# Optimization experiments

Measured on AMD Instinct MI355X. Metric: run time of the kernel, lower is better.

Reference implementation:

```python
import jax, jax.numpy as jnp
import numpy as np

N = 40000      # num nodes
M = 640000     # num edges (avg degree 16)
D = 128        # hidden_size / embed_dim
H = 8          # attn_num_heads
HD = D // H    # head_dim = 16
FF = 512       # tfmr_ff_sz
LN_EPS = 1e-5
SOFTMAX_EPS = 1e-16  # matches torch_geometric.utils.softmax


def setup_inputs() -> dict:
    key = jax.random.key(0)
    ks = jax.random.split(key, 8)
    s = 0.05
    return {
        "node_states": jax.random.normal(ks[0], (N, D), dtype=jnp.float32),
        "edges": jax.random.randint(ks[1], (2, M), 0, N, dtype=jnp.int64),
        # SelfAttentionMessageLayer params (F.linear convention: W is (out, in))
        "w_qkv": jax.random.normal(ks[2], (3 * D, D), dtype=jnp.float32) * s,
        "b_qkv": jnp.zeros((3 * D,), dtype=jnp.float32),
        "w_out": jax.random.normal(ks[3], (D, D), dtype=jnp.float32) * s,
        "b_out": jnp.zeros((D,), dtype=jnp.float32),
        # TransformerUpdateLayer params
        "w1": jax.random.normal(ks[4], (FF, D), dtype=jnp.float32) * s,
        "b1": jnp.zeros((FF,), dtype=jnp.float32),
        "w2": jax.random.normal(ks[5], (D, FF), dtype=jnp.float32) * s,
        "b2": jnp.zeros((D,), dtype=jnp.float32),
        "g1": jnp.ones((D,), dtype=jnp.float32),
        "beta1": jnp.zeros((D,), dtype=jnp.float32),
        "g2": jnp.ones((D,), dtype=jnp.float32),
        "beta2": jnp.zeros((D,), dtype=jnp.float32),
    }


def _layer_norm(x, g, b):
    mu = jnp.mean(x, axis=-1, keepdims=True)
    var = jnp.mean(jnp.square(x - mu), axis=-1, keepdims=True)
    return g * (x - mu) * jax.lax.rsqrt(var + LN_EPS) + b


def _sparse_self_attention(node_states, edges, w_qkv, b_qkv, w_out, b_out):
    num_nodes = node_states.shape[0]
    src, tgt = edges[0], edges[1]
    qkv = node_states @ w_qkv.T + b_qkv                      # (N, 3D)
    q, k, v = jnp.split(qkv, 3, axis=1)                      # each (N, D)
    q_e = q[tgt]                                             # (M, D) gather by target
    k_e = k[src]                                             # (M, D) gather by source
    v_e = v[src]                                             # (M, D)
    m = q_e.shape[0]
    # per-edge, per-head scaled dot-product scores
    scores = (q_e * k_e).reshape(m, H, HD).sum(-1) * (HD ** -0.5)   # (M, H)
    # scatter-softmax over edges sharing the same target node
    smax = jax.ops.segment_max(scores, tgt, num_segments=num_nodes)  # (N, H)
    smax = jnp.where(jnp.isfinite(smax), smax, 0.0)                  # empty segments
    ex = jnp.exp(scores - smax[tgt])                                 # (M, H)
    ssum = jax.ops.segment_sum(ex, tgt, num_segments=num_nodes)      # (N, H)
    attn_w = ex / (ssum[tgt] + SOFTMAX_EPS)                          # (M, H)
    # weighted scatter-add aggregation
    msg = (v_e.reshape(m, H, HD) * attn_w[:, :, None]).reshape(m, D)  # (M, D)
    agg = jax.ops.segment_sum(msg, tgt, num_segments=num_nodes)      # (N, D)
    return agg @ w_out.T + b_out


def _update(messages, node_states, w1, b1, w2, b2, g1, beta1, g2, beta2):
    x = _layer_norm(node_states + messages, g1, beta1)
    ff = jax.nn.relu(x @ w1.T + b1) @ w2.T + b2
    return _layer_norm(x + ff, g2, beta2)


def reference(node_states, edges, w_qkv, b_qkv, w_out, b_out,
              w1, b1, w2, b2, g1, beta1, g2, beta2):
    old_node_states = node_states
    # layer_timesteps = [1]: one message/update layer, one propagation step
    messages = _sparse_self_attention(node_states, edges, w_qkv, b_qkv, w_out, b_out)
    node_states = _update(messages, node_states, w1, b1, w2, b2, g1, beta1, g2, beta2)
    return (node_states, old_node_states)
```

## Files before the change

### kernel.cpp

```cpp
#include <hip/hip_runtime.h>
#include <hip/hip_bf16.h>
#include <math.h>

#define D_DIM 128
#define FF_DIM 512
#define BSTRIDE 64
#define BCAP 63
#define PSHIFT 6
#define NBINS 625
#define CAP_BIN 1280
#define P1_EPB 4096

typedef __attribute__((ext_vector_type(8))) short bf16x8;
typedef __attribute__((ext_vector_type(4))) float f32x4;
typedef __attribute__((ext_vector_type(2))) float f32x2;
typedef __attribute__((ext_vector_type(4))) unsigned short u16x4;

__device__ __forceinline__ short f2bf(float f) {
    union { float f; unsigned u; } x; x.f = f;
    unsigned r = x.u + 0x7FFF + ((x.u >> 16) & 1);
    return (short)(r >> 16);
}
__device__ __forceinline__ float bf2f(short s) {
    union { unsigned u; float f; } x;
    x.u = ((unsigned)(unsigned short)s) << 16;
    return x.f;
}
__device__ __forceinline__ float lof(unsigned u) {
    union { unsigned u; float f; } x; x.u = u << 16; return x.f;
}
__device__ __forceinline__ float hif(unsigned u) {
    union { unsigned u; float f; } x; x.u = u & 0xFFFF0000u; return x.f;
}
__device__ __forceinline__ unsigned char f2fp8(float v) {
    return (unsigned char)(__builtin_amdgcn_cvt_pk_fp8_f32(v, v, 0, false) & 0xFF);
}

__device__ __forceinline__ void load_lds16(const short* g, short* l) {
    __builtin_amdgcn_global_load_lds(
        (const __attribute__((address_space(1))) unsigned int*)g,
        (__attribute__((address_space(3))) unsigned int*)l, 16, 0, 0);
}

template<int OUT_BF16, int RELU>
__global__ __launch_bounds__(256) void gemm_mfma(
    const short* __restrict__ A, const short* __restrict__ B,
    const float* __restrict__ bias, void* __restrict__ C,
    int Nc, int K)
{
    __shared__ short lA[2][128 * 32];
    __shared__ short lB[2][128 * 32];

    const int tid  = threadIdx.x;
    const int lane = tid & 63;
    const int wave = tid >> 6;
    const int wr = wave >> 1, wc = wave & 1;
    const int row0 = blockIdx.y * 128;
    const int col0 = blockIdx.x * 128;
    const int fr = lane & 15;
    const int fq = lane >> 4;
    const int sw = (fr >> 1) & 3;
    const int rdoff = (fq ^ sw) * 8;

    const int c0c = tid,        r0 = c0c >> 2, qg0 = (c0c & 3) ^ ((r0 >> 1) & 3);
    const int c1c = 256 + tid,  r1 = c1c >> 2, qg1 = (c1c & 3) ^ ((r1 >> 1) & 3);

#define STAGE_G(buf, kk) { \
    load_lds16(A + (size_t)(row0 + r0) * K + (kk) + qg0 * 8, &lA[buf][c0c * 8]); \
    load_lds16(B + (size_t)(col0 + r0) * K + (kk) + qg0 * 8, &lB[buf][c0c * 8]); \
    load_lds16(A + (size_t)(row0 + r1) * K + (kk) + qg1 * 8, &lA[buf][c1c * 8]); \
    load_lds16(B + (size_t)(col0 + r1) * K + (kk) + qg1 * 8, &lB[buf][c1c * 8]); }

    f32x4 acc[4][4] = {};
    const int nk = K >> 5;

    STAGE_G(0, 0)
    __syncthreads();
    int cur = 0;
    for (int t = 0; t < nk; ++t) {
        if (t + 1 < nk) STAGE_G(cur ^ 1, (t + 1) * 32)

        bf16x8 af[4], bfr[4];
#pragma unroll
        for (int m = 0; m < 4; ++m)
            af[m] = *(const bf16x8*)&lA[cur][(wr * 64 + m * 16 + fr) * 32 + rdoff];
#pragma unroll
        for (int n2 = 0; n2 < 4; ++n2)
            bfr[n2] = *(const bf16x8*)&lB[cur][(wc * 64 + n2 * 16 + fr) * 32 + rdoff];
#pragma unroll
        for (int m = 0; m < 4; ++m)
#pragma unroll
            for (int n2 = 0; n2 < 4; ++n2)
                acc[m][n2] = __builtin_amdgcn_mfma_f32_16x16x32_bf16(
                    af[m], bfr[n2], acc[m][n2], 0, 0, 0);
        __syncthreads();
        cur ^= 1;
    }
#undef STAGE_G

#pragma unroll
    for (int m = 0; m < 4; ++m) {
        int r = row0 + wr * 64 + m * 16 + fq * 4;
#pragma unroll
        for (int n2 = 0; n2 < 4; ++n2) {
            int c = col0 + wc * 64 + n2 * 16 + fr;
            float bb = bias[c];
#pragma unroll
            for (int j = 0; j < 4; ++j) {
                float v = acc[m][n2][j] + bb;
                if (RELU) v = fmaxf(v, 0.0f);
                if (OUT_BF16)
                    ((short*)C)[(size_t)(r + j) * Nc + c] = f2bf(v);
                else
                    ((float*)C)[(size_t)(r + j) * Nc + c] = v;
            }
        }
    }
}

__global__ __launch_bounds__(256) void qkv_bucket(
    const short* __restrict__ A, const short* __restrict__ B,
    const float* __restrict__ bias, void* __restrict__ C, int K,
    const unsigned* __restrict__ part, const int* __restrict__ gcur,
    int* __restrict__ csr, int ngemm)
{
    __shared__ short lA[2][128 * 32];
    __shared__ short lB[2][128 * 32];
    __shared__ int lbkt[64 * BSTRIDE];
    __shared__ int lcnt[64];

    const int b = blockIdx.x;
    const int tid = threadIdx.x;

    if (b >= ngemm) {
        int bin = b - ngemm;
        for (int i = tid; i < 64; i += 256) lcnt[i] = 0;
        __syncthreads();
        int cnt = gcur[bin]; if (cnt > CAP_BIN) cnt = CAP_BIN;
        const unsigned* pp = part + (size_t)bin * CAP_BIN;
        for (int i = tid; i < cnt; i += 256) {
            unsigned pk = pp[i];
            int lt = (pk >> 16) & 63;
            int s  = pk & 0xFFFF;
            int pos = atomicAdd(&lcnt[lt], 1);
            if (pos < BCAP) lbkt[lt * BSTRIDE + 1 + pos] = s;
        }
        __syncthreads();
        for (int i = tid; i < 64; i += 256) lbkt[i * BSTRIDE] = lcnt[i];
        __syncthreads();
        int4* dst = (int4*)(csr + (size_t)bin * 64 * BSTRIDE);
        const int4* sp = (const int4*)lbkt;
        for (int i = tid; i < 64 * BSTRIDE / 4; i += 256) dst[i] = sp[i];
        return;
    }

    const int lane = tid & 63;
    const int wave = tid >> 6;
    const int wr = wave >> 1, wc = wave & 1;
    const int row0 = (b / 3) * 128;
    const int col0 = (b % 3) * 128;
    const int fr = lane & 15;
    const int fq = lane >> 4;
    const int sw = (fr >> 1) & 3;
    const int rdoff = (fq ^ sw) * 8;

    const int c0c = tid,        r0 = c0c >> 2, qg0 = (c0c & 3) ^ ((r0 >> 1) & 3);
    const int c1c = 256 + tid,  r1 = c1c >> 2, qg1 = (c1c & 3) ^ ((r1 >> 1) & 3);

#define STAGE_Q(buf, kk) { \
    load_lds16(A + (size_t)(row0 + r0) * K + (kk) + qg0 * 8, &lA[buf][c0c * 8]); \
    load_lds16(B + (size_t)(col0 + r0) * K + (kk) + qg0 * 8, &lB[buf][c0c * 8]); \
    load_lds16(A + (size_t)(row0 + r1) * K + (kk) + qg1 * 8, &lA[buf][c1c * 8]); \
    load_lds16(B + (size_t)(col0 + r1) * K + (kk) + qg1 * 8, &lB[buf][c1c * 8]); }

    f32x4 acc[4][4] = {};
    const int nk = K >> 5;

    STAGE_Q(0, 0)
    __syncthreads();
    int cur = 0;
    for (int t = 0; t < nk; ++t) {
        if (t + 1 < nk) STAGE_Q(cur ^ 1, (t + 1) * 32)

        bf16x8 af[4], bfr[4];
#pragma unroll
        for (int m = 0; m < 4; ++m)
            af[m] = *(const bf16x8*)&lA[cur][(wr * 64 + m * 16 + fr) * 32 + rdoff];
#pragma unroll
        for (int n2 = 0; n2 < 4; ++n2)
            bfr[n2] = *(const bf16x8*)&lB[cur][(wc * 64 + n2 * 16 + fr) * 32 + rdoff];
#pragma unroll
        for (int m = 0; m < 4; ++m)
#pragma unroll
            for (int n2 = 0; n2 < 4; ++n2)
                acc[m][n2] = __builtin_amdgcn_mfma_f32_16x16x32_bf16(
                    af[m], bfr[n2], acc[m][n2], 0, 0, 0);
        __syncthreads();
        cur ^= 1;
    }
#undef STAGE_Q

#pragma unroll
    for (int m = 0; m < 4; ++m) {
        int r = row0 + wr * 64 + m * 16 + fq * 4;
#pragma unroll
        for (int n2 = 0; n2 < 4; ++n2) {
            int c = col0 + wc * 64 + n2 * 16 + fr;
            float bb = bias[c];
#pragma unroll
            for (int j = 0; j < 4; ++j) {
                float v = acc[m][n2][j] + bb;
                if (col0 == 0) {
                    ((short*)C)[(size_t)(r + j) * 256 + c] = f2bf(v);
                } else {
                    size_t byteoff = (size_t)(r + j) * 512 +
                        (col0 == 128 ? 256 + (c - 128) : 384 + (c - 256));
                    ((unsigned char*)C)[byteoff] = f2fp8(v);
                }
            }
        }
    }
}

template<int KD, int RES_BF, int OUT_BF>
__global__ __launch_bounds__(256) void gemm_ln(
    const short* __restrict__ A, const short* __restrict__ B,
    const float* __restrict__ bias, const void* __restrict__ res,
    const float* __restrict__ gamma, const float* __restrict__ beta,
    float* __restrict__ out32, short* __restrict__ outbf, int n)
{
    __shared__ short lA[2][64 * 32];
    __shared__ short lB[2][128 * 32];
    __shared__ float sums[64][2], sqs[64][2];
    __shared__ float muA[64], rsA[64];

    const int tid  = threadIdx.x;
    const int lane = tid & 63;
    const int wave = tid >> 6;
    const int wr = wave >> 1, wc = wave & 1;
    const int row0 = blockIdx.x * 64;
    const int fr = lane & 15;
    const int fq = lane >> 4;
    const int sw = (fr >> 1) & 3;
    const int rdoff = (fq ^ sw) * 8;

    const int ra = tid >> 2,        qa = (tid & 3) ^ ((ra >> 1) & 3);
    const int cb0 = tid,       rb0 = cb0 >> 2, qb0 = (cb0 & 3) ^ ((rb0 >> 1) & 3);
    const int cb1 = 256 + tid, rb1 = cb1 >> 2, qb1 = (cb1 & 3) ^ ((rb1 >> 1) & 3);

#define STAGE_L(buf, kk) { \
    load_lds16(A + (size_t)(row0 + ra) * KD + (kk) + qa * 8,  &lA[buf][tid * 8]); \
    load_lds16(B + (size_t)rb0 * KD + (kk) + qb0 * 8, &lB[buf][cb0 * 8]); \
    load_lds16(B + (size_t)rb1 * KD + (kk) + qb1 * 8, &lB[buf][cb1 * 8]); }

    f32x4 acc[2][4] = {};
    const int nk = KD >> 5;

    STAGE_L(0, 0)
    __syncthreads();
    int cur = 0;
    for (int t = 0; t < nk; ++t) {
        if (t + 1 < nk) STAGE_L(cur ^ 1, (t + 1) * 32)

        bf16x8 af[2], bfr[4];
#pragma unroll
        for (int m = 0; m < 2; ++m)
            af[m] = *(const bf16x8*)&lA[cur][(wr * 32 + m * 16 + fr) * 32 + rdoff];
#pragma unroll
        for (int n2 = 0; n2 < 4; ++n2)
            bfr[n2] = *(const bf16x8*)&lB[cur][(wc * 64 + n2 * 16 + fr) * 32 + rdoff];
#pragma unroll
        for (int m = 0; m < 2; ++m)
#pragma unroll
            for (int n2 = 0; n2 < 4; ++n2)
                acc[m][n2] = __builtin_amdgcn_mfma_f32_16x16x32_bf16(
                    af[m], bfr[n2], acc[m][n2], 0, 0, 0);
        __syncthreads();
        cur ^= 1;
    }
#undef STAGE_L

    float bicol[4], gcol[4], bcol[4];
#pragma unroll
    for (int n2 = 0; n2 < 4; ++n2) {
        int c = wc * 64 + n2 * 16 + fr;
        bicol[n2] = bias[c]; gcol[n2] = gamma[c]; bcol[n2] = beta[c];
    }

#pragma unroll
    for (int m = 0; m < 2; ++m) {
#pragma unroll
        for (int j = 0; j < 4; ++j) {
            int rl = wr * 32 + m * 16 + fq * 4 + j;
            int rg = row0 + rl;
            float ps = 0.0f, pq = 0.0f;
#pragma unroll
            for (int n2 = 0; n2 < 4; ++n2) {
                float v = acc[m][n2][j] + bicol[n2];
                if (rg < n) {
                    size_t ri = (size_t)rg * 128 + wc * 64 + n2 * 16 + fr;
                    v += RES_BF ? bf2f(((const short*)res)[ri])
                                : ((const float*)res)[ri];
                }
                acc[m][n2][j] = v;
                ps += v; pq += v * v;
            }
            ps += __shfl_xor(ps, 1); ps += __shfl_xor(ps, 2);
            ps += __shfl_xor(ps, 4); ps += __shfl_xor(ps, 8);
            pq += __shfl_xor(pq, 1); pq += __shfl_xor(pq, 2);
            pq += __shfl_xor(pq, 4); pq += __shfl_xor(pq, 8);
            if (fr == 0) { sums[rl][wc] = ps; sqs[rl][wc] = pq; }
        }
    }
    __syncthreads();
    if (tid < 64) {
        float s = sums[tid][0] + sums[tid][1];
        float q = sqs[tid][0] + sqs[tid][1];
        float mu = s * (1.0f / 128.0f);
        float var = q * (1.0f / 128.0f) - mu * mu;
        muA[tid] = mu;
        rsA[tid] = rsqrtf(var + 1e-5f);
    }
    __syncthreads();

#pragma unroll
    for (int m = 0; m < 2; ++m) {
#pragma unroll
        for (int j = 0; j < 4; ++j) {
            int rl = wr * 32 + m * 16 + fq * 4 + j;
            int rg = row0 + rl;
            float mu = muA[rl], rs = rsA[rl];
#pragma unroll
            for (int n2 = 0; n2 < 4; ++n2) {
                int c = wc * 64 + n2 * 16 + fr;
                float o = gcol[n2] * (acc[m][n2][j] - mu) * rs + bcol[n2];
                if (OUT_BF) {
                    outbf[(size_t)rg * 128 + c] = (rg < n) ? f2bf(o) : (short)0;
                } else {
                    if (rg < n) out32[(size_t)rg * 128 + c] = o;
                }
            }
        }
    }
}

__global__ __launch_bounds__(256) void prep_kernel(
    const float* __restrict__ ns, short* __restrict__ nsbf,
    float* __restrict__ out_old, int n_elems, int mp_elems,
    const float* w0, const float* w1, const float* w2, const float* w3,
    short* o0, short* o1, short* o2, short* o3,
    int c0, int c1, int c2, int c3,
    const int* __restrict__ e_src, const int* __restrict__ e_tgt,
    int* __restrict__ gcur, unsigned* __restrict__ part,
    int m_edges, int nconv)
{
    __shared__ int hist[NBINS];
    __shared__ int base[NBINS];

    const int tid = threadIdx.x;

    if (blockIdx.x >= nconv) {
        int pblk = blockIdx.x - nconv;
        int e0 = pblk * P1_EPB;
        for (int i = tid; i < NBINS; i += 256) hist[i] = 0;
        __syncthreads();
        unsigned packs[16]; int bins[16];
#pragma unroll
        for (int j = 0; j < 16; ++j) {
            int i = e0 + j * 256 + tid;
            if (i < m_edges) {
                int t = e_tgt[i], s = e_src[i];
                packs[j] = ((unsigned)t << 16) | (unsigned)s;
                bins[j] = t >> PSHIFT;
                atomicAdd(&hist[bins[j]], 1);
            } else { bins[j] = -1; packs[j] = 0u; }
        }
        __syncthreads();
        for (int i = tid; i < NBINS; i += 256) {
            int c = hist[i];
            base[i] = c ? atomicAdd(&gcur[i], c) : 0;
            hist[i] = 0;
        }
        __syncthreads();
#pragma unroll
        for (int j = 0; j < 16; ++j) {
            if (bins[j] >= 0) {
                int pos = base[bins[j]] + atomicAdd(&hist[bins[j]], 1);
                if (pos < CAP_BIN)
                    part[(size_t)bins[j] * CAP_BIN + pos] = packs[j];
            }
        }
        return;
    }

    int i = blockIdx.x * 256 + tid;
    int i4 = i * 4;
    if (i4 < mp_elems) {
        if (i4 < n_elems) {
            float4 v = *(const float4*)(ns + i4);
            *(float4*)(out_old + i4) = v;
            u16x4 b;
            b.x = (unsigned short)f2bf(v.x); b.y = (unsigned short)f2bf(v.y);
            b.z = (unsigned short)f2bf(v.z); b.w = (unsigned short)f2bf(v.w);
            *(u16x4*)(nsbf + i4) = b;
        } else {
            u16x4 z = {0, 0, 0, 0};
            *(u16x4*)(nsbf + i4) = z;
        }
    }
    if (i < c0) o0[i] = f2bf(w0[i]);
    if (i < c1) o1[i] = f2bf(w1[i]);
    if (i < c2) o2[i] = f2bf(w2[i]);
    if (i < c3) o3[i] = f2bf(w3[i]);
}

template<int NG>
__device__ __forceinline__ void attn_fast(
    int cnt, int e, int mysrc,
    const unsigned char* kb, const unsigned char* vb,
    f32x2 q01, f32x2 q23, f32x2 q45, f32x2 q67,
    float& l, f32x2& A01, f32x2& A23, f32x2& A45, f32x2& A67)
{
    uint2 kr[NG]; float sc[NG]; int si[NG];
#pragma unroll
    for (int G = 0; G < NG; ++G) {
        if (4 * G < cnt) {
            int idx = 4 * G + e; if (idx >= cnt) idx = cnt - 1;
            si[G] = __shfl(mysrc, idx);
            kr[G] = *(const uint2*)(kb + (size_t)si[G] * 512);
        }
    }
    float mloc = -INFINITY;
#pragma unroll
    for (int G = 0; G < NG; ++G) {
        if (4 * G < cnt) {
            f32x2 s2 = q01 * __builtin_amdgcn_cvt_pk_f32_fp8(kr[G].x, 0);
            s2 += q23 * __builtin_amdgcn_cvt_pk_f32_fp8(kr[G].x, 1);
            s2 += q45 * __builtin_amdgcn_cvt_pk_f32_fp8(kr[G].y, 0);
            s2 += q67 * __builtin_amdgcn_cvt_pk_f32_fp8(kr[G].y, 1);
            float s = s2.x + s2.y;
            s += __shfl_xor(s, 4);
            sc[G] = (4 * G + e < cnt) ? s : -INFINITY;
            mloc = fmaxf(mloc, sc[G]);
        }
    }
    mloc = fmaxf(mloc, __shfl_xor(mloc, 1));
    mloc = fmaxf(mloc, __shfl_xor(mloc, 2));
#pragma unroll
    for (int G = 0; G < NG; ++G) {
        if (4 * G < cnt) {
            float p = exp2f(sc[G] - mloc);
            sc[G] = p;
            l += p;
        }
    }
    uint2 vr[NG];
#pragma unroll
    for (int G = 0; G < NG; ++G) {
        if (4 * G < cnt)
            vr[G] = *(const uint2*)(vb + (size_t)si[G] * 512);
    }
#pragma unroll
    for (int G = 0; G < NG; ++G) {
        if (4 * G < cnt) {
            f32x2 pv = {sc[G], sc[G]};
            A01 += pv * __builtin_amdgcn_cvt_pk_f32_fp8(vr[G].x, 0);
            A23 += pv * __builtin_amdgcn_cvt_pk_f32_fp8(vr[G].x, 1);
            A45 += pv * __builtin_amdgcn_cvt_pk_f32_fp8(vr[G].y, 0);
            A67 += pv * __builtin_amdgcn_cvt_pk_f32_fp8(vr[G].y, 1);
        }
    }
}

__global__ __launch_bounds__(256) void attn_kernel(
    const short* __restrict__ qkv, const int* __restrict__ csr,
    short* __restrict__ agg, int n, int mp)
{
    int node = blockIdx.x * 4 + (threadIdx.x >> 6);
    int lane = threadIdx.x & 63;
    if (node >= mp) return;
    const int hh = lane >> 2;
    const int e  = lane & 3;
    unsigned* outp = (unsigned*)(agg + (size_t)node * 128 + hh * 8 + e * 2);

    const int* bkt = csr + (size_t)node * BSTRIDE;
    int cnt = 0;
    if (node < n) {
        cnt = bkt[0];
        if (cnt > BCAP) cnt = BCAP;
    }
    if (cnt == 0) { *outp = 0u; return; }

    const float SC = 0.25f * 1.44269504088896340736f;
    const uint4 qd = *(const uint4*)(qkv + (size_t)node * 256 + hh * 8);
    f32x2 q01 = {lof(qd.x) * SC, hif(qd.x) * SC};
    f32x2 q23 = {lof(qd.y) * SC, hif(qd.y) * SC};
    f32x2 q45 = {lof(qd.z) * SC, hif(qd.z) * SC};
    f32x2 q67 = {lof(qd.w) * SC, hif(qd.w) * SC};

    const unsigned char* kb = (const unsigned char*)qkv + 256 + hh * 8;
    const unsigned char* vb = (const unsigned char*)qkv + 384 + hh * 8;

    float l = 0.0f;
    f32x2 A01 = {0, 0}, A23 = {0, 0}, A45 = {0, 0}, A67 = {0, 0};

    int mysrc = bkt[1 + ((lane < cnt) ? lane : (cnt - 1))];

    if (cnt <= 16) {
        attn_fast<4>(cnt, e, mysrc, kb, vb, q01, q23, q45, q67,
                     l, A01, A23, A45, A67);
    } else if (cnt <= 32) {
        attn_fast<8>(cnt, e, mysrc, kb, vb, q01, q23, q45, q67,
                     l, A01, A23, A45, A67);
    } else {
        float m = -INFINITY;
        uint2 kA, vA;
        {
            int sA = bkt[1 + ((e < cnt) ? e : 0)];
            kA = *(const uint2*)(kb + (size_t)sA * 512);
            vA = *(const uint2*)(vb + (size_t)sA * 512);
        }
        for (int g = 0; g < cnt; g += 4) {
            uint2 kB = kA, vB = vA;
            if (g + 4 < cnt) {
                int t = g + 4 + e;
                int sB = bkt[1 + ((t < cnt) ? t : 0)];
                kB = *(const uint2*)(kb + (size_t)sB * 512);
                vB = *(const uint2*)(vb + (size_t)sB * 512);
            }
            f32x2 s2 = q01 * __builtin_amdgcn_cvt_pk_f32_fp8(kA.x, 0);
            s2 += q23 * __builtin_amdgcn_cvt_pk_f32_fp8(kA.x, 1);
            s2 += q45 * __builtin_amdgcn_cvt_pk_f32_fp8(kA.y, 0);
            s2 += q67 * __builtin_amdgcn_cvt_pk_f32_fp8(kA.y, 1);
            float s = s2.x + s2.y;
            s += __shfl_xor(s, 4);
            float scv = (g + e < cnt) ? s : -INFINITY;
            float gm = fmaxf(scv, __shfl_xor(scv, 1));
            gm = fmaxf(gm, __shfl_xor(gm, 2));
            float mnew = fmaxf(m, gm);
            float corr = exp2f(m - mnew);
            float p = exp2f(scv - mnew);
            l = fmaf(l, corr, p);
            f32x2 cv = {corr, corr}, pv = {p, p};
            A01 = A01 * cv + pv * __builtin_amdgcn_cvt_pk_f32_fp8(vA.x, 0);
            A23 = A23 * cv + pv * __builtin_amdgcn_cvt_pk_f32_fp8(vA.x, 1);
            A45 = A45 * cv + pv * __builtin_amdgcn_cvt_pk_f32_fp8(vA.y, 0);
            A67 = A67 * cv + pv * __builtin_amdgcn_cvt_pk_f32_fp8(vA.y, 1);
            m = mnew;
            kA = kB; vA = vB;
        }
    }

    float a0 = A01.x, a1 = A01.y, a2 = A23.x, a3 = A23.y;
    float a4 = A45.x, a5 = A45.y, a6 = A67.x, a7 = A67.y;

    l  += __shfl_xor(l, 1);
    a0 += __shfl_xor(a0, 1); a1 += __shfl_xor(a1, 1);
    a2 += __shfl_xor(a2, 1); a3 += __shfl_xor(a3, 1);
    a4 += __shfl_xor(a4, 1); a5 += __shfl_xor(a5, 1);
    a6 += __shfl_xor(a6, 1); a7 += __shfl_xor(a7, 1);
    l  += __shfl_xor(l, 2);
    a0 += __shfl_xor(a0, 2); a1 += __shfl_xor(a1, 2);
    a2 += __shfl_xor(a2, 2); a3 += __shfl_xor(a3, 2);
    a4 += __shfl_xor(a4, 2); a5 += __shfl_xor(a5, 2);
    a6 += __shfl_xor(a6, 2); a7 += __shfl_xor(a7, 2);

    float inv = 1.0f / l;
    float o0, o1;
    if (e == 0)      { o0 = a0; o1 = a1; }
    else if (e == 1) { o0 = a2; o1 = a3; }
    else if (e == 2) { o0 = a4; o1 = a5; }
    else             { o0 = a6; o1 = a7; }
    *outp = ((unsigned)(unsigned short)f2bf(o1 * inv) << 16) |
            (unsigned)(unsigned short)f2bf(o0 * inv);
}

extern "C" void kernel_launch(void* const* d_in, const int* in_sizes, int n_in,
                              void* d_out, int out_size, void* d_ws, size_t ws_size,
                              hipStream_t stream)
{
    const float* node_states = (const float*)d_in[0];
    const int*   edges       = (const int*)d_in[1];
    const float* w_qkv = (const float*)d_in[2];
    const float* b_qkv = (const float*)d_in[3];
    const float* w_out = (const float*)d_in[4];
    const float* b_out = (const float*)d_in[5];
    const float* w1    = (const float*)d_in[6];
    const float* b1    = (const float*)d_in[7];
    const float* w2    = (const float*)d_in[8];
    const float* b2    = (const float*)d_in[9];
    const float* g1    = (const float*)d_in[10];
    const float* beta1 = (const float*)d_in[11];
    const float* g2    = (const float*)d_in[12];
    const float* beta2 = (const float*)d_in[13];

    const int N  = in_sizes[0] / D_DIM;
    const int M  = in_sizes[1] / 2;
    const int MP = ((N + 127) / 128) * 128;
    const int* e_src = edges;
    const int* e_tgt = edges + M;

    float* out_new = (float*)d_out;
    float* out_old = (float*)d_out + (size_t)N * D_DIM;

    size_t off = 0;
    auto alloc = [&](size_t bytes) -> void* {
        void* p = (char*)d_ws + off;
        off += (bytes + 255) & ~(size_t)255;
        return p;
    };
    short* ns_bf   = (short*)alloc((size_t)MP * D_DIM * 2);
    char*  region  = (char*)alloc((size_t)MP * 512);
    short* qkv_pk  = (short*)region;
    short* xbuf_bf = (short*)region;
    short* agg_bf  = (short*)alloc((size_t)MP * D_DIM * 2);
    short* ff1_bf  = (short*)alloc((size_t)MP * FF_DIM * 2);
    short* wqkv_bf = (short*)alloc((size_t)384 * 128 * 2);
    short* wout_bf = (short*)alloc((size_t)128 * 128 * 2);
    short* w1_bf   = (short*)alloc((size_t)512 * 128 * 2);
    short* w2_bf   = (short*)alloc((size_t)128 * 512 * 2);
    int* csr       = (int*)alloc((size_t)N * BSTRIDE * 4);
    unsigned* part = (unsigned*)alloc((size_t)NBINS * CAP_BIN * 4);
    int* gcur      = (int*)alloc((size_t)NBINS * 4);
    (void)ws_size;

    hipMemsetAsync(gcur, 0, (size_t)NBINS * 4, stream);

    const int nconv = (MP * D_DIM / 4 + 255) / 256;
    const int nP1   = (M + P1_EPB - 1) / P1_EPB;
    prep_kernel<<<nconv + nP1, 256, 0, stream>>>(
        node_states, ns_bf, out_old, N * D_DIM, MP * D_DIM,
        w_qkv, w_out, w1, w2, wqkv_bf, wout_bf, w1_bf, w2_bf,
        384 * 128, 128 * 128, 512 * 128, 128 * 512,
        e_src, e_tgt, gcur, part, M, nconv);

    {
        const int ngemm = 3 * (MP / 128);
        qkv_bucket<<<ngemm + NBINS, 256, 0, stream>>>(
            ns_bf, wqkv_bf, b_qkv, qkv_pk, 128,
            part, gcur, csr, ngemm);
    }
    attn_kernel<<<MP / 4, 256, 0, stream>>>(qkv_pk, csr, agg_bf, N, MP);
    gemm_ln<128, 1, 1><<<MP / 64, 256, 0, stream>>>(
        agg_bf, wout_bf, b_out, ns_bf, g1, beta1,
        (float*)nullptr, xbuf_bf, N);
    {
        dim3 grid(FF_DIM / 128, MP / 128);
        gemm_mfma<1, 1><<<grid, 256, 0, stream>>>(xbuf_bf, w1_bf, b1,
                                                  ff1_bf, FF_DIM, 128);
    }
    gemm_ln<512, 1, 0><<<MP / 64, 256, 0, stream>>>(
        ff1_bf, w2_bf, b2, xbuf_bf, g2, beta2, out_new, (short*)nullptr, N);
}
```

Measured before the change: 149.7 us.

## Fuse out-projection+LayerNorm with FF1 GEMM and split Q/KV buffers

Merges the W_out GEMM + residual + LayerNorm kernel with the following FF1 GEMM+ReLU. The normalized rows are kept in a swizzled LDS tile and multiplied by W1, which is read directly from global memory. This removes one kernel launch and the global read of the intermediate x buffer. It also splits the packed QKV buffer into a bf16 Q array and a compact 256-byte-stride fp8 K/V array, so attention gathers touch denser rows. The cost is extra LDS per block and unstaged W1 fragment loads from global/L2.

```diff
diff --git a/kernel.cpp b/kernel.cpp
--- a/kernel.cpp
+++ b/kernel.cpp
@@ -42,85 +42,10 @@
         (__attribute__((address_space(3))) unsigned int*)l, 16, 0, 0);
 }
 
-template<int OUT_BF16, int RELU>
-__global__ __launch_bounds__(256) void gemm_mfma(
-    const short* __restrict__ A, const short* __restrict__ B,
-    const float* __restrict__ bias, void* __restrict__ C,
-    int Nc, int K)
-{
-    __shared__ short lA[2][128 * 32];
-    __shared__ short lB[2][128 * 32];
-
-    const int tid  = threadIdx.x;
-    const int lane = tid & 63;
-    const int wave = tid >> 6;
-    const int wr = wave >> 1, wc = wave & 1;
-    const int row0 = blockIdx.y * 128;
-    const int col0 = blockIdx.x * 128;
-    const int fr = lane & 15;
-    const int fq = lane >> 4;
-    const int sw = (fr >> 1) & 3;
-    const int rdoff = (fq ^ sw) * 8;
-
-    const int c0c = tid,        r0 = c0c >> 2, qg0 = (c0c & 3) ^ ((r0 >> 1) & 3);
-    const int c1c = 256 + tid,  r1 = c1c >> 2, qg1 = (c1c & 3) ^ ((r1 >> 1) & 3);
-
-#define STAGE_G(buf, kk) { \
-    load_lds16(A + (size_t)(row0 + r0) * K + (kk) + qg0 * 8, &lA[buf][c0c * 8]); \
-    load_lds16(B + (size_t)(col0 + r0) * K + (kk) + qg0 * 8, &lB[buf][c0c * 8]); \
-    load_lds16(A + (size_t)(row0 + r1) * K + (kk) + qg1 * 8, &lA[buf][c1c * 8]); \
-    load_lds16(B + (size_t)(col0 + r1) * K + (kk) + qg1 * 8, &lB[buf][c1c * 8]); }
-
-    f32x4 acc[4][4] = {};
-    const int nk = K >> 5;
-
-    STAGE_G(0, 0)
-    __syncthreads();
-    int cur = 0;
-    for (int t = 0; t < nk; ++t) {
-        if (t + 1 < nk) STAGE_G(cur ^ 1, (t + 1) * 32)
-
-        bf16x8 af[4], bfr[4];
-#pragma unroll
-        for (int m = 0; m < 4; ++m)
-            af[m] = *(const bf16x8*)&lA[cur][(wr * 64 + m * 16 + fr) * 32 + rdoff];
-#pragma unroll
-        for (int n2 = 0; n2 < 4; ++n2)
-            bfr[n2] = *(const bf16x8*)&lB[cur][(wc * 64 + n2 * 16 + fr) * 32 + rdoff];
-#pragma unroll
-        for (int m = 0; m < 4; ++m)
-#pragma unroll
-            for (int n2 = 0; n2 < 4; ++n2)
-                acc[m][n2] = __builtin_amdgcn_mfma_f32_16x16x32_bf16(
-                    af[m], bfr[n2], acc[m][n2], 0, 0, 0);
-        __syncthreads();
-        cur ^= 1;
-    }
-#undef STAGE_G
-
-#pragma unroll
-    for (int m = 0; m < 4; ++m) {
-        int r = row0 + wr * 64 + m * 16 + fq * 4;
-#pragma unroll
-        for (int n2 = 0; n2 < 4; ++n2) {
-            int c = col0 + wc * 64 + n2 * 16 + fr;
-            float bb = bias[c];
-#pragma unroll
-            for (int j = 0; j < 4; ++j) {
-                float v = acc[m][n2][j] + bb;
-                if (RELU) v = fmaxf(v, 0.0f);
-                if (OUT_BF16)
-                    ((short*)C)[(size_t)(r + j) * Nc + c] = f2bf(v);
-                else
-                    ((float*)C)[(size_t)(r + j) * Nc + c] = v;
-            }
-        }
-    }
-}
-
 __global__ __launch_bounds__(256) void qkv_bucket(
     const short* __restrict__ A, const short* __restrict__ B,
-    const float* __restrict__ bias, void* __restrict__ C, int K,
+    const float* __restrict__ bias, short* __restrict__ Q,
+    unsigned char* __restrict__ KV, int K,
     const unsigned* __restrict__ part, const int* __restrict__ gcur,
     int* __restrict__ csr, int ngemm)
 {
@@ -211,28 +136,30 @@
             for (int j = 0; j < 4; ++j) {
                 float v = acc[m][n2][j] + bb;
                 if (col0 == 0) {
-                    ((short*)C)[(size_t)(r + j) * 256 + c] = f2bf(v);
+                    Q[(size_t)(r + j) * 128 + c] = f2bf(v);
+                } else if (col0 == 128) {
+                    KV[(size_t)(r + j) * 256 + (c - 128)] = f2fp8(v);
                 } else {
-                    size_t byteoff = (size_t)(r + j) * 512 +
-                        (col0 == 128 ? 256 + (c - 128) : 384 + (c - 256));
-                    ((unsigned char*)C)[byteoff] = f2fp8(v);
+                    KV[(size_t)(r + j) * 256 + 128 + (c - 256)] = f2fp8(v);
                 }
             }
         }
     }
 }
 
-template<int KD, int RES_BF, int OUT_BF>
-__global__ __launch_bounds__(256) void gemm_ln(
+__global__ __launch_bounds__(256) void wout_ln_ff1(
     const short* __restrict__ A, const short* __restrict__ B,
-    const float* __restrict__ bias, const void* __restrict__ res,
+    const float* __restrict__ bias, const short* __restrict__ res,
     const float* __restrict__ gamma, const float* __restrict__ beta,
-    float* __restrict__ out32, short* __restrict__ outbf, int n)
+    short* __restrict__ outbf,
+    const short* __restrict__ W1, const float* __restrict__ b1,
+    short* __restrict__ ff1, int n)
 {
     __shared__ short lA[2][64 * 32];
     __shared__ short lB[2][128 * 32];
     __shared__ float sums[64][2], sqs[64][2];
     __shared__ float muA[64], rsA[64];
+    __shared__ short xl[64 * 128];
 
     const int tid  = threadIdx.x;
     const int lane = tid & 63;
@@ -249,18 +176,17 @@
     const int cb1 = 256 + tid, rb1 = cb1 >> 2, qb1 = (cb1 & 3) ^ ((rb1 >> 1) & 3);
 
 #define STAGE_L(buf, kk) { \
-    load_lds16(A + (size_t)(row0 + ra) * KD + (kk) + qa * 8,  &lA[buf][tid * 8]); \
-    load_lds16(B + (size_t)rb0 * KD + (kk) + qb0 * 8, &lB[buf][cb0 * 8]); \
-    load_lds16(B + (size_t)rb1 * KD + (kk) + qb1 * 8, &lB[buf][cb1 * 8]); }
+    load_lds16(A + (size_t)(row0 + ra) * 128 + (kk) + qa * 8,  &lA[buf][tid * 8]); \
+    load_lds16(B + (size_t)rb0 * 128 + (kk) + qb0 * 8, &lB[buf][cb0 * 8]); \
+    load_lds16(B + (size_t)rb1 * 128 + (kk) + qb1 * 8, &lB[buf][cb1 * 8]); }
 
     f32x4 acc[2][4] = {};
-    const int nk = KD >> 5;
 
     STAGE_L(0, 0)
     __syncthreads();
     int cur = 0;
-    for (int t = 0; t < nk; ++t) {
-        if (t + 1 < nk) STAGE_L(cur ^ 1, (t + 1) * 32)
+    for (int t = 0; t < 4; ++t) {
+        if (t + 1 < 4) STAGE_L(cur ^ 1, (t + 1) * 32)
 
         bf16x8 af[2], bfr[4];
 #pragma unroll
@@ -297,11 +223,8 @@
 #pragma unroll
             for (int n2 = 0; n2 < 4; ++n2) {
                 float v = acc[m][n2][j] + bicol[n2];
-                if (rg < n) {
-                    size_t ri = (size_t)rg * 128 + wc * 64 + n2 * 16 + fr;
-                    v += RES_BF ? bf2f(((const short*)res)[ri])
-                                : ((const float*)res)[ri];
-                }
+                if (rg < n)
+                    v += bf2f(res[(size_t)rg * 128 + wc * 64 + n2 * 16 + fr]);
                 acc[m][n2][j] = v;
                 ps += v; pq += v * v;
             }
@@ -334,11 +257,166 @@
             for (int n2 = 0; n2 < 4; ++n2) {
                 int c = wc * 64 + n2 * 16 + fr;
                 float o = gcol[n2] * (acc[m][n2][j] - mu) * rs + bcol[n2];
-                if (OUT_BF) {
-                    outbf[(size_t)rg * 128 + c] = (rg < n) ? f2bf(o) : (short)0;
-                } else {
-                    if (rg < n) out32[(size_t)rg * 128 + c] = o;
+                short ob = (rg < n) ? f2bf(o) : (short)0;
+                outbf[(size_t)rg * 128 + c] = ob;
+                int c8s = ((c >> 3) ^ (rl & 7));
+                xl[rl * 128 + (c8s << 3) + (c & 7)] = ob;
+            }
+        }
+    }
+    __syncthreads();
+
+    for (int cc = 0; cc < 4; ++cc) {
+        const int c0 = wc * 256 + cc * 64;
+        f32x4 a2[2][4] = {};
+#pragma unroll
+        for (int ks = 0; ks < 4; ++ks) {
+            int k0 = ks * 32;
+            bf16x8 af[2], bfr[4];
+#pragma unroll
+            for (int m = 0; m < 2; ++m) {
+                int row = wr * 32 + m * 16 + fr;
+                int ch = ((k0 >> 3) + fq) ^ (row & 7);
+                af[m] = *(const bf16x8*)&xl[row * 128 + (ch << 3)];
+            }
+#pragma unroll
+            for (int n2 = 0; n2 < 4; ++n2)
+                bfr[n2] = *(const bf16x8*)(W1 + (size_t)(c0 + n2 * 16 + fr) * 128
+                                              + k0 + fq * 8);
+#pragma unroll
+            for (int m = 0; m < 2; ++m)
+#pragma unroll
+                for (int n2 = 0; n2 < 4; ++n2)
+                    a2[m][n2] = __builtin_amdgcn_mfma_f32_16x16x32_bf16(
+                        af[m], bfr[n2], a2[m][n2], 0, 0, 0);
+        }
+#pragma unroll
+        for (int m = 0; m < 2; ++m) {
+#pragma unroll
+            for (int n2 = 0; n2 < 4; ++n2) {
+                int c = c0 + n2 * 16 + fr;
+                float bb = b1[c];
+#pragma unroll
+                for (int j = 0; j < 4; ++j) {
+                    int rg = row0 + wr * 32 + m * 16 + fq * 4 + j;
+                    float v = fmaxf(a2[m][n2][j] + bb, 0.0f);
+                    ff1[(size_t)rg * 512 + c] = f2bf(v);
                 }
+            }
+        }
+    }
+}
+
+template<int KD>
+__global__ __launch_bounds__(256) void gemm_ln(
+    const short* __restrict__ A, const short* __restrict__ B,
+    const float* __restrict__ bias, const short* __restrict__ res,
+    const float* __restrict__ gamma, const float* __restrict__ beta,
+    float* __restrict__ out32, int n)
+{
+    __shared__ short lA[2][64 * 32];
+    __shared__ short lB[2][128 * 32];
+    __shared__ float sums[64][2], sqs[64][2];
+    __shared__ float muA[64], rsA[64];
+
+    const int tid  = threadIdx.x;
+    const int lane = tid & 63;
+    const int wave = tid >> 6;
+    const int wr = wave >> 1, wc = wave & 1;
+    const int row0 = blockIdx.x * 64;
+    const int fr = lane & 15;
+    const int fq = lane >> 4;
+    const int sw = (fr >> 1) & 3;
+    const int rdoff = (fq ^ sw) * 8;
+
+    const int ra = tid >> 2,        qa = (tid & 3) ^ ((ra >> 1) & 3);
+    const int cb0 = tid,       rb0 = cb0 >> 2, qb0 = (cb0 & 3) ^ ((rb0 >> 1) & 3);
+    const int cb1 = 256 + tid, rb1 = cb1 >> 2, qb1 = (cb1 & 3) ^ ((rb1 >> 1) & 3);
+
+#define STAGE_L(buf, kk) { \
+    load_lds16(A + (size_t)(row0 + ra) * KD + (kk) + qa * 8,  &lA[buf][tid * 8]); \
+    load_lds16(B + (size_t)rb0 * KD + (kk) + qb0 * 8, &lB[buf][cb0 * 8]); \
+    load_lds16(B + (size_t)rb1 * KD + (kk) + qb1 * 8, &lB[buf][cb1 * 8]); }
+
+    f32x4 acc[2][4] = {};
+    const int nk = KD >> 5;
+
+    STAGE_L(0, 0)
+    __syncthreads();
+    int cur = 0;
+    for (int t = 0; t < nk; ++t) {
+        if (t + 1 < nk) STAGE_L(cur ^ 1, (t + 1) * 32)
+
+        bf16x8 af[2], bfr[4];
+#pragma unroll
+        for (int m = 0; m < 2; ++m)
+            af[m] = *(const bf16x8*)&lA[cur][(wr * 32 + m * 16 + fr) * 32 + rdoff];
+#pragma unroll
+        for (int n2 = 0; n2 < 4; ++n2)
+            bfr[n2] = *(const bf16x8*)&lB[cur][(wc * 64 + n2 * 16 + fr) * 32 + rdoff];
+#pragma unroll
+        for (int m = 0; m < 2; ++m)
+#pragma unroll
+            for (int n2 = 0; n2 < 4; ++n2)
+                acc[m][n2] = __builtin_amdgcn_mfma_f32_16x16x32_bf16(
+                    af[m], bfr[n2], acc[m][n2], 0, 0, 0);
+        __syncthreads();
+        cur ^= 1;
+    }
+#undef STAGE_L
+
+    float bicol[4], gcol[4], bcol[4];
+#pragma unroll
+    for (int n2 = 0; n2 < 4; ++n2) {
+        int c = wc * 64 + n2 * 16 + fr;
+        bicol[n2] = bias[c]; gcol[n2] = gamma[c]; bcol[n2] = beta[c];
+    }
+
+#pragma unroll
+    for (int m = 0; m < 2; ++m) {
+#pragma unroll
+        for (int j = 0; j < 4; ++j) {
+            int rl = wr * 32 + m * 16 + fq * 4 + j;
+            int rg = row0 + rl;
+            float ps = 0.0f, pq = 0.0f;
+#pragma unroll
+            for (int n2 = 0; n2 < 4; ++n2) {
+                float v = acc[m][n2][j] + bicol[n2];
+                if (rg < n)
+                    v += bf2f(res[(size_t)rg * 128 + wc * 64 + n2 * 16 + fr]);
+                acc[m][n2][j] = v;
+                ps += v; pq += v * v;
+            }
+            ps += __shfl_xor(ps, 1); ps += __shfl_xor(ps, 2);
+            ps += __shfl_xor(ps, 4); ps += __shfl_xor(ps, 8);
+            pq += __shfl_xor(pq, 1); pq += __shfl_xor(pq, 2);
+            pq += __shfl_xor(pq, 4); pq += __shfl_xor(pq, 8);
+            if (fr == 0) { sums[rl][wc] = ps; sqs[rl][wc] = pq; }
+        }
+    }
+    __syncthreads();
+    if (tid < 64) {
+        float s = sums[tid][0] + sums[tid][1];
+        float q = sqs[tid][0] + sqs[tid][1];
+        float mu = s * (1.0f / 128.0f);
+        float var = q * (1.0f / 128.0f) - mu * mu;
+        muA[tid] = mu;
+        rsA[tid] = rsqrtf(var + 1e-5f);
+    }
+    __syncthreads();
+
+#pragma unroll
+    for (int m = 0; m < 2; ++m) {
+#pragma unroll
+        for (int j = 0; j < 4; ++j) {
+            int rl = wr * 32 + m * 16 + fq * 4 + j;
+            int rg = row0 + rl;
+            float mu = muA[rl], rs = rsA[rl];
+#pragma unroll
+            for (int n2 = 0; n2 < 4; ++n2) {
+                int c = wc * 64 + n2 * 16 + fr;
+                float o = gcol[n2] * (acc[m][n2][j] - mu) * rs + bcol[n2];
+                if (rg < n) out32[(size_t)rg * 128 + c] = o;
             }
         }
     }
@@ -427,7 +505,7 @@
         if (4 * G < cnt) {
             int idx = 4 * G + e; if (idx >= cnt) idx = cnt - 1;
             si[G] = __shfl(mysrc, idx);
-            kr[G] = *(const uint2*)(kb + (size_t)si[G] * 512);
+            kr[G] = *(const uint2*)(kb + (size_t)si[G] * 256);
         }
     }
     float mloc = -INFINITY;
@@ -458,7 +536,7 @@
 #pragma unroll
     for (int G = 0; G < NG; ++G) {
         if (4 * G < cnt)
-            vr[G] = *(const uint2*)(vb + (size_t)si[G] * 512);
+            vr[G] = *(const uint2*)(vb + (size_t)si[G] * 256);
     }
 #pragma unroll
     for (int G = 0; G < NG; ++G) {
@@ -473,8 +551,8 @@
 }
 
 __global__ __launch_bounds__(256) void attn_kernel(
-    const short* __restrict__ qkv, const int* __restrict__ csr,
-    short* __restrict__ agg, int n, int mp)
+    const short* __restrict__ qb, const unsigned char* __restrict__ kv8,
+    const int* __restrict__ csr, short* __restrict__ agg, int n, int mp)
 {
     int node = blockIdx.x * 4 + (threadIdx.x >> 6);
     int lane = threadIdx.x & 63;
@@ -492,14 +570,14 @@
     if (cnt == 0) { *outp = 0u; return; }
 
     const float SC = 0.25f * 1.44269504088896340736f;
-    const uint4 qd = *(const uint4*)(qkv + (size_t)node * 256 + hh * 8);
+    const uint4 qd = *(const uint4*)(qb + (size_t)node * 128 + hh * 8);
     f32x2 q01 = {lof(qd.x) * SC, hif(qd.x) * SC};
     f32x2 q23 = {lof(qd.y) * SC, hif(qd.y) * SC};
     f32x2 q45 = {lof(qd.z) * SC, hif(qd.z) * SC};
     f32x2 q67 = {lof(qd.w) * SC, hif(qd.w) * SC};
 
-    const unsigned char* kb = (const unsigned char*)qkv + 256 + hh * 8;
-    const unsigned char* vb = (const unsigned char*)qkv + 384 + hh * 8;
+    const unsigned char* kb = kv8 + hh * 8;
+    const unsigned char* vb = kv8 + 128 + hh * 8;
 
     float l = 0.0f;
     f32x2 A01 = {0, 0}, A23 = {0, 0}, A45 = {0, 0}, A67 = {0, 0};
@@ -517,16 +595,16 @@
         uint2 kA, vA;
         {
             int sA = bkt[1 + ((e < cnt) ? e : 0)];
-            kA = *(const uint2*)(kb + (size_t)sA * 512);
-            vA = *(const uint2*)(vb + (size_t)sA * 512);
+            kA = *(const uint2*)(kb + (size_t)sA * 256);
+            vA = *(const uint2*)(vb + (size_t)sA * 256);
         }
         for (int g = 0; g < cnt; g += 4) {
             uint2 kB = kA, vB = vA;
             if (g + 4 < cnt) {
                 int t = g + 4 + e;
                 int sB = bkt[1 + ((t < cnt) ? t : 0)];
-                kB = *(const uint2*)(kb + (size_t)sB * 512);
-                vB = *(const uint2*)(vb + (size_t)sB * 512);
+                kB = *(const uint2*)(kb + (size_t)sB * 256);
+                vB = *(const uint2*)(vb + (size_t)sB * 256);
             }
             f32x2 s2 = q01 * __builtin_amdgcn_cvt_pk_f32_fp8(kA.x, 0);
             s2 += q23 * __builtin_amdgcn_cvt_pk_f32_fp8(kA.x, 1);
@@ -610,9 +688,9 @@
         return p;
     };
     short* ns_bf   = (short*)alloc((size_t)MP * D_DIM * 2);
-    char*  region  = (char*)alloc((size_t)MP * 512);
-    short* qkv_pk  = (short*)region;
-    short* xbuf_bf = (short*)region;
+    short* qb      = (short*)alloc((size_t)MP * D_DIM * 2);
+    short* xbuf_bf = qb;
+    unsigned char* kv8 = (unsigned char*)alloc((size_t)MP * 256);
     short* agg_bf  = (short*)alloc((size_t)MP * D_DIM * 2);
     short* ff1_bf  = (short*)alloc((size_t)MP * FF_DIM * 2);
     short* wqkv_bf = (short*)alloc((size_t)384 * 128 * 2);
@@ -637,18 +715,13 @@
     {
         const int ngemm = 3 * (MP / 128);
         qkv_bucket<<<ngemm + NBINS, 256, 0, stream>>>(
-            ns_bf, wqkv_bf, b_qkv, qkv_pk, 128,
+            ns_bf, wqkv_bf, b_qkv, qb, kv8, 128,
             part, gcur, csr, ngemm);
     }
-    attn_kernel<<<MP / 4, 256, 0, stream>>>(qkv_pk, csr, agg_bf, N, MP);
-    gemm_ln<128, 1, 1><<<MP / 64, 256, 0, stream>>>(
-        agg_bf, wout_bf, b_out, ns_bf, g1, beta1,
-        (float*)nullptr, xbuf_bf, N);
-    {
-        dim3 grid(FF_DIM / 128, MP / 128);
-        gemm_mfma<1, 1><<<grid, 256, 0, stream>>>(xbuf_bf, w1_bf, b1,
-                                                  ff1_bf, FF_DIM, 128);
-    }
-    gemm_ln<512, 1, 0><<<MP / 64, 256, 0, stream>>>(
-        ff1_bf, w2_bf, b2, xbuf_bf, g2, beta2, out_new, (short*)nullptr, N);
-}
+    attn_kernel<<<MP / 4, 256, 0, stream>>>(qb, kv8, csr, agg_bf, N, MP);
+    wout_ln_ff1<<<MP / 64, 256, 0, stream>>>(
+        agg_bf, wout_bf, b_out, ns_bf, g1, beta1, xbuf_bf,
+        w1_bf, b1, ff1_bf, N);
+    gemm_ln<512><<<MP / 64, 256, 0, stream>>>(
+        ff1_bf, w2_bf, b2, xbuf_bf, g2, beta2, out_new, N);
+}
```

Result: slower. 162.7 us (+8.7%).
